# Performance work log

Measured on AMD Instinct MI355X. Metric: run time of the kernel, lower is better.

The kernel has to match this reference:

```python
import jax, jax.numpy as jnp
import numpy as np

K_HOPS = 3
N_NODES = 50000
N_EDGES = 800000
N_FEAT = 256
N_CLASS = 64


def setup_inputs() -> dict:
    key = jax.random.key(0)
    k1, k2, k3, k4 = jax.random.split(key, 4)
    x = jax.random.normal(k1, (N_NODES, N_FEAT), dtype=jnp.float32)
    edge_index = jax.random.randint(k2, (2, N_EDGES), 0, N_NODES, dtype=jnp.int64)
    # Linear(nfeat -> nclass) params, Glorot-ish init
    W = jax.random.normal(k3, (N_FEAT, N_CLASS), dtype=jnp.float32) / np.sqrt(N_FEAT)
    b = jnp.zeros((N_CLASS,), dtype=jnp.float32)
    return {"x": x, "edge_index": edge_index, "W": W, "b": b}


def reference(x, edge_index, W, b):
    # SGC: out = (D^-1/2 (A+I) D^-1/2)^K x  @ W + b
    N = x.shape[0]
    self_idx = jnp.arange(N, dtype=edge_index.dtype)
    src = jnp.concatenate([edge_index[0], self_idx])  # [E+N]
    dst = jnp.concatenate([edge_index[1], self_idx])  # [E+N]
    deg = jax.ops.segment_sum(jnp.ones_like(dst, dtype=x.dtype), dst, num_segments=N)
    dinv = jnp.where(deg > 0, jax.lax.rsqrt(deg), 0.0)
    norm = dinv[src] * dinv[dst]  # [E+N] per-edge coefficient
    for _ in range(K_HOPS):
        # gather source features, scale, scatter-add into destinations
        x = jax.ops.segment_sum(x[src] * norm[:, None], dst, num_segments=N)
    return x @ W + b
```

## Files before the change

### kernel.cpp

```cpp
#include <hip/hip_runtime.h>
#include <hip/hip_bf16.h>


#define NFEAT 256
#define NCLS  64
#define ELLW  64
#define NPB   128
#define BCAP  4096
#define PCHUNK 8192

typedef __attribute__((ext_vector_type(8))) short bf16x8;
typedef __attribute__((ext_vector_type(4))) float f32x4;
typedef __attribute__((ext_vector_type(2))) float f32x2;
typedef __attribute__((ext_vector_type(4))) int   i32x4;
typedef __attribute__((ext_vector_type(4))) unsigned int u32x4;

__device__ __forceinline__ float bf2f(unsigned int u) {
    return __uint_as_float(u << 16);
}
__device__ __forceinline__ float bf2f_hi(unsigned int u) {
    return __uint_as_float(u & 0xffff0000u);
}
__device__ __forceinline__ unsigned short f2bf(float f) {
    unsigned int u = __float_as_uint(f);
    unsigned int r = u + 0x7fffu + ((u >> 16) & 1u);
    return (unsigned short)(r >> 16);
}
__device__ __forceinline__ unsigned int pack2bf(float a, float b) {
    return (unsigned int)f2bf(a) | ((unsigned int)f2bf(b) << 16);
}

__global__ void k_setup(const void* ei, int twoE, int nnodes,
                        const unsigned int* __restrict__ x, int nwords,
                        const void* __restrict__ Wg, const void* __restrict__ Bg,
                        int* flag, int* fflag, int* gcur, int NB,
                        unsigned short* __restrict__ Wt, float* __restrict__ bc) {
    __shared__ int acc;
    const int t = threadIdx.x;
    const int b = blockIdx.x;
    if (t == 0) acc = 0;
    __syncthreads();

    if (b == 0) {
        const long long* p = (const long long*)ei;
        int nchk = 2048;
        if (nchk > twoE / 2) nchk = twoE / 2;
        int bad = 0;
        for (int i = t; i < nchk; i += 256) {
            long long v = p[i];
            if (v < 0 || v >= (long long)nnodes) bad++;
        }
        if (bad) atomicAdd(&acc, bad);
        __syncthreads();
        if (t == 0) *flag = (acc == 0) ? 1 : 0;
        return;
    }

    int lim = nwords < 4096 ? nwords : 4096;
    int wild = 0;
    for (int i = t; i < lim; i += 256) {
        unsigned int lo = x[i] & 0xffffu;
        unsigned int expf = (lo >> 7) & 0xffu;
        if (expf >= 0x97u) wild++;
    }
    if (wild) atomicAdd(&acc, wild);
    __syncthreads();
    const bool isbf = (acc < 8);

    if (b == 1) {
        if (t == 0) *fflag = isbf ? 1 : 0;
        for (int i = t; i < NB; i += 256) gcur[i] = 0;
        if (t < NCLS) {
            bc[t] = isbf ? bf2f(((const unsigned short*)Bg)[t])
                         : ((const float*)Bg)[t];
        }
        return;
    }

    int i = (b - 2) * 256 + t;
    if (i < NFEAT * NCLS) {
        int n = i >> 8, k = i & 255;
        Wt[i] = isbf ? ((const unsigned short*)Wg)[k * NCLS + n]
                     : f2bf(((const float*)Wg)[k * NCLS + n]);
    }
}

__launch_bounds__(256)
__global__ void k_fused(const void* __restrict__ Xg,
                        const unsigned short* __restrict__ Wt,
                        unsigned short* __restrict__ Yb,
                        int N, int NB, const int* __restrict__ fflag,
                        const void* __restrict__ ei, int E, const int* __restrict__ flag,
                        unsigned int* __restrict__ bucket, int* __restrict__ gcur,
                        int ngemm) {
    __shared__ char smem[32768 + 3 * 1600];
    const int t = threadIdx.x;

    if (blockIdx.x >= ngemm) {
        unsigned int* stage = (unsigned int*)smem;
        int* hist = (int*)(smem + 32768);
        int* base = hist + 400;
        int* rank = base + 400;
        for (int b = t; b < NB; b += 256) { hist[b] = 0; rank[b] = 0; }
        __syncthreads();
        const int bstart = (blockIdx.x - ngemm) * PCHUNK;
        const bool is64 = (*flag != 0);
#pragma unroll
        for (int i = 0; i < PCHUNK / 256; ++i) {
            int e = bstart + i * 256 + t;
            unsigned int v = 0xFFFFFFFFu;
            if (e < E) {
                int ss, dd;
                if (is64) {
                    ss = (int)__builtin_nontemporal_load((const long long*)ei + e);
                    dd = (int)__builtin_nontemporal_load((const long long*)ei + E + e);
                } else {
                    ss = __builtin_nontemporal_load((const int*)ei + e);
                    dd = __builtin_nontemporal_load((const int*)ei + E + e);
                }
                int j = dd >> 7;
                atomicAdd(&hist[j], 1);
                v = ((unsigned int)j << 23) | ((unsigned int)(dd & 127) << 16) |
                    (unsigned int)ss;
            }
            stage[i * 256 + t] = v;
        }
        __syncthreads();
        for (int b = t; b < NB; b += 256) base[b] = atomicAdd(&gcur[b], hist[b]);
        __syncthreads();
#pragma unroll
        for (int i = 0; i < PCHUNK / 256; ++i) {
            unsigned int v = stage[i * 256 + t];
            if (v != 0xFFFFFFFFu) {
                int j = v >> 23;
                int r = atomicAdd(&rank[j], 1);
                int pos = base[j] + r;
                if (pos < BCAP)
                    bucket[(size_t)j * BCAP + pos] = v & 0x7FFFFFu;
            }
        }
        return;
    }

    unsigned short* Ws = (unsigned short*)smem;
    for (int it = 0; it < 8; ++it) {
        int idx = t + 256 * it;
        int lane_e = idx & 63;
        int nt = (idx >> 6) & 3;
        int ks = idx >> 8;
        int n = nt * 16 + (lane_e & 15);
        int k = ks * 32 + (lane_e >> 4) * 8;
        const unsigned short* srcp = Wt + n * 256 + k;
        ushort4 v0 = *(const ushort4*)srcp;
        ushort4 v1 = *(const ushort4*)(srcp + 4);
        unsigned short* dstp = &Ws[idx * 8];
        *(ushort4*)dstp = v0;
        *(ushort4*)(dstp + 4) = v1;
    }
    __syncthreads();

    const int wv = t >> 6, lane = t & 63;
    const int m = lane & 15, q = lane >> 4;
    const int row = blockIdx.x * 64 + wv * 16 + m;
    const bool rowok = row < N;
    const bool isbf = (*fflag != 0);

    f32x4 acc0 = {0.f, 0.f, 0.f, 0.f};
    f32x4 acc1 = {0.f, 0.f, 0.f, 0.f};
    f32x4 acc2 = {0.f, 0.f, 0.f, 0.f};
    f32x4 acc3 = {0.f, 0.f, 0.f, 0.f};

    for (int ks = 0; ks < 8; ++ks) {
        const int kk = ks * 32 + q * 8;
        bf16x8 af = {0, 0, 0, 0, 0, 0, 0, 0};
        if (rowok) {
            if (isbf) {
                const i32x4* xp = (const i32x4*)((const unsigned short*)Xg + (size_t)row * NFEAT + kk);
                i32x4 raw = __builtin_nontemporal_load(xp);
#pragma unroll
                for (int h = 0; h < 4; ++h) {
                    af[2 * h]     = (short)(raw[h] & 0xffff);
                    af[2 * h + 1] = (short)(((unsigned int)raw[h]) >> 16);
                }
            } else {
                const i32x4* xp = (const i32x4*)((const float*)Xg + (size_t)row * NFEAT + kk);
                i32x4 r0 = __builtin_nontemporal_load(xp);
                i32x4 r1 = __builtin_nontemporal_load(xp + 1);
#pragma unroll
                for (int h = 0; h < 4; ++h) {
                    af[h]     = (short)f2bf(__int_as_float(r0[h]));
                    af[h + 4] = (short)f2bf(__int_as_float(r1[h]));
                }
            }
        }
        const unsigned short* wbase = &Ws[(ks * 4) * 512 + lane * 8];
        bf16x8 b0 = *(const bf16x8*)(wbase);
        bf16x8 b1 = *(const bf16x8*)(wbase + 512);
        bf16x8 b2 = *(const bf16x8*)(wbase + 1024);
        bf16x8 b3 = *(const bf16x8*)(wbase + 1536);
        acc0 = __builtin_amdgcn_mfma_f32_16x16x32_bf16(af, b0, acc0, 0, 0, 0);
        acc1 = __builtin_amdgcn_mfma_f32_16x16x32_bf16(af, b1, acc1, 0, 0, 0);
        acc2 = __builtin_amdgcn_mfma_f32_16x16x32_bf16(af, b2, acc2, 0, 0, 0);
        acc3 = __builtin_amdgcn_mfma_f32_16x16x32_bf16(af, b3, acc3, 0, 0, 0);
    }

    const int rowbase = blockIdx.x * 64 + wv * 16 + q * 4;
#pragma unroll
    for (int i = 0; i < 4; ++i) {
        int gr = rowbase + i;
        if (gr < N) {
            unsigned short* yp = Yb + (size_t)gr * NCLS + m;
            yp[0]  = f2bf(acc0[i]);
            yp[16] = f2bf(acc1[i]);
            yp[32] = f2bf(acc2[i]);
            yp[48] = f2bf(acc3[i]);
        }
    }
}

__launch_bounds__(256)
__global__ void k_build(const unsigned int* __restrict__ bucket,
                        const int* __restrict__ gcur,
                        int* __restrict__ cnt, float* __restrict__ dinv,
                        unsigned short* __restrict__ ellu,
                        const unsigned int* __restrict__ Yb,
                        unsigned int* __restrict__ Zlo,
                        unsigned int* __restrict__ Zhi,
                        int N) {
    __shared__ unsigned short ellb[NPB * ELLW];
    __shared__ int lcnt[NPB];
    __shared__ float sdinv[NPB];
    const int t = threadIdx.x;
    const int j = blockIdx.x;
    if (t < NPB) lcnt[t] = 0;
    {
        u32x4* eb4 = (u32x4*)ellb;
        u32x4 z = {0, 0, 0, 0};
        for (int i = t; i < NPB * ELLW / 8; i += 256) eb4[i] = z;
    }
    __syncthreads();
    int total = gcur[j];
    if (total > BCAP) total = BCAP;
    const unsigned int* bb = bucket + (size_t)j * BCAP;
    for (int i = t; i < total; i += 256) {
        unsigned int v = __builtin_nontemporal_load(bb + i);
        int ld = (v >> 16) & 127;
        int s = v & 0xffffu;
        int r = atomicAdd(&lcnt[ld], 1);
        if (r < ELLW) ellb[(ld << 6) + r] = (unsigned short)s;
    }
    __syncthreads();
    const int node0 = j << 7;
    if (t < NPB) {
        int node = node0 + t;
        int c = lcnt[t];
        float dv = rsqrtf((float)(c + 1));
        sdinv[t] = dv;
        if (node < N) {
            cnt[node] = c > ELLW ? ELLW : c;
            dinv[node] = dv;
        }
    }
    __syncthreads();
    u32x4* ellg = (u32x4*)ellu;
    const u32x4* eb = (const u32x4*)ellb;
    for (int i = t; i < NPB * (ELLW / 8); i += 256) {
        int node = node0 + (i >> 3);
        if (node < N) ellg[(size_t)node0 * 8 + i] = eb[i];
    }
    for (int w = t; w < NPB * 32; w += 256) {
        int nl = w >> 5, l = w & 31;
        int node = node0 + nl;
        if (node < N) {
            float dv = sdinv[nl];
            unsigned int y = Yb[(size_t)node * 32 + l];
            unsigned int zz = pack2bf(dv * bf2f(y), dv * bf2f_hi(y));
            if (l < 16) Zlo[(size_t)node * 16 + l] = zz;
            else        Zhi[(size_t)node * 16 + (l - 16)] = zz;
        }
    }
}

__launch_bounds__(256)
__global__ void k_hop(const unsigned int* __restrict__ Zlo_in,
                      const unsigned int* __restrict__ Zhi_in,
                      const unsigned short* __restrict__ ellu,
                      const int* __restrict__ cnt, const float* __restrict__ dinv,
                      unsigned int* __restrict__ Zlo_out,
                      unsigned int* __restrict__ Zhi_out,
                      float* __restrict__ outf,
                      const float* __restrict__ bc, int N) {
    const int half = blockIdx.x & 1;
    const int node = (blockIdx.x >> 1) * 16 + (threadIdx.x >> 4);
    if (node >= N) return;
    const int l = threadIdx.x & 15;
    const unsigned int* __restrict__ Zin = half ? Zhi_in : Zlo_in;

    const int deg = __builtin_nontemporal_load(cnt + node);
    const float dn = __builtin_nontemporal_load(dinv + node);
    unsigned int zself = Zin[node * 16 + l];
    float a0 = bf2f(zself), a1 = 0.f, a2 = 0.f, a3 = 0.f;
    float b0 = bf2f_hi(zself), b1 = 0.f, b2 = 0.f, b3 = 0.f;
    const unsigned short* erow = ellu + (size_t)node * ELLW;
    int e = 0;
    for (; e + 16 <= deg; e += 16) {
        u32x4 ua = __builtin_nontemporal_load((const u32x4*)(erow + e));
        u32x4 ub = __builtin_nontemporal_load((const u32x4*)(erow + e) + 1);
        int s[16];
#pragma unroll
        for (int i = 0; i < 4; ++i) {
            s[2 * i]     = (int)(ua[i] & 0xffffu);
            s[2 * i + 1] = (int)(ua[i] >> 16);
            s[2 * i + 8] = (int)(ub[i] & 0xffffu);
            s[2 * i + 9] = (int)(ub[i] >> 16);
        }
        unsigned int z[16];
#pragma unroll
        for (int i = 0; i < 16; ++i) z[i] = Zin[s[i] * 16 + l];
#pragma unroll
        for (int i = 0; i < 16; i += 4) {
            a0 += bf2f(z[i]);     b0 += bf2f_hi(z[i]);
            a1 += bf2f(z[i + 1]); b1 += bf2f_hi(z[i + 1]);
            a2 += bf2f(z[i + 2]); b2 += bf2f_hi(z[i + 2]);
            a3 += bf2f(z[i + 3]); b3 += bf2f_hi(z[i + 3]);
        }
    }
    if (e < deg) {
        u32x4 ua = __builtin_nontemporal_load((const u32x4*)(erow + e));
        u32x4 ub = __builtin_nontemporal_load((const u32x4*)(erow + e) + 1);
        int s[16];
#pragma unroll
        for (int i = 0; i < 4; ++i) {
            s[2 * i]     = (int)(ua[i] & 0xffffu);
            s[2 * i + 1] = (int)(ua[i] >> 16);
            s[2 * i + 8] = (int)(ub[i] & 0xffffu);
            s[2 * i + 9] = (int)(ub[i] >> 16);
        }
        unsigned int z[16];
#pragma unroll
        for (int i = 0; i < 16; ++i) z[i] = Zin[s[i] * 16 + l];
#pragma unroll
        for (int i = 0; i < 16; i += 4) {
            bool g0 = (e + i < deg), g1 = (e + i + 1 < deg);
            bool g2 = (e + i + 2 < deg), g3 = (e + i + 3 < deg);
            a0 += g0 ? bf2f(z[i]) : 0.f;     b0 += g0 ? bf2f_hi(z[i]) : 0.f;
            a1 += g1 ? bf2f(z[i + 1]) : 0.f; b1 += g1 ? bf2f_hi(z[i + 1]) : 0.f;
            a2 += g2 ? bf2f(z[i + 2]) : 0.f; b2 += g2 ? bf2f_hi(z[i + 2]) : 0.f;
            a3 += g3 ? bf2f(z[i + 3]) : 0.f; b3 += g3 ? bf2f_hi(z[i + 3]) : 0.f;
        }
    }
    float lo = (a0 + a1) + (a2 + a3);
    float hi = (b0 + b1) + (b2 + b3);
    if (outf) {
        float2 bv = *(const float2*)(bc + half * 32 + 2 * l);
        f32x2 o = {dn * lo + bv.x, dn * hi + bv.y};
        __builtin_nontemporal_store(o, (f32x2*)(outf + (size_t)node * NCLS + half * 32 + 2 * l));
    } else {
        unsigned int* __restrict__ Zout = half ? Zhi_out : Zlo_out;
        float d2 = dn * dn;
        __builtin_nontemporal_store(pack2bf(d2 * lo, d2 * hi), Zout + (size_t)node * 16 + l);
    }
}

extern "C" void kernel_launch(void* const* d_in, const int* in_sizes, int n_in,
                              void* d_out, int out_size, void* d_ws, size_t ws_size,
                              hipStream_t stream) {
    const void* X  = d_in[0];
    const void* EI = d_in[1];
    const void* W  = d_in[2];
    const void* B  = d_in[3];
    float* out = (float*)d_out;

    const int N = in_sizes[0] / NFEAT;
    const int twoE = in_sizes[1];
    const int E = twoE / 2;
    const int NB = (N + NPB - 1) / NPB;

    char* p = (char*)d_ws;
    auto alloc = [&](size_t bytes) -> char* {
        char* q = p;
        p += (bytes + 255) & ~(size_t)255;
        return q;
    };
    int*   flag   = (int*)alloc(4);
    int*   fflag  = (int*)alloc(4);
    int*   gcur   = (int*)alloc((size_t)NB * 4);
    int*   cnt    = (int*)alloc((size_t)N * 4);
    float* dinv   = (float*)alloc((size_t)N * 4);
    unsigned short* Wt = (unsigned short*)alloc((size_t)NFEAT * NCLS * 2);
    float* bc     = (float*)alloc((size_t)NCLS * 4);
    unsigned int* bucket = (unsigned int*)alloc((size_t)NB * BCAP * 4);
    unsigned short* ellu = (unsigned short*)alloc((size_t)N * ELLW * 2);
    unsigned short* Y0 = (unsigned short*)alloc((size_t)N * NCLS * 2);
    unsigned int* Zlo0 = (unsigned int*)alloc((size_t)N * 16 * 4);
    unsigned int* Zlo1 = (unsigned int*)alloc((size_t)N * 16 * 4);
    unsigned int* Zhi0 = (unsigned int*)alloc((size_t)N * 16 * 4);
    unsigned int* Zhi1 = (unsigned int*)alloc((size_t)N * 16 * 4);

    k_setup<<<2 + NFEAT * NCLS / 256, 256, 0, stream>>>(
        EI, twoE, N, (const unsigned int*)X, in_sizes[0] / 2,
        W, B, flag, fflag, gcur, NB, Wt, bc);

    const int ngemm = (N + 63) / 64;
    const int npart = (E + PCHUNK - 1) / PCHUNK;
    k_fused<<<ngemm + npart, 256, 0, stream>>>(X, Wt, Y0, N, NB, fflag,
                                               EI, E, flag, bucket, gcur, ngemm);

    k_build<<<NB, 256, 0, stream>>>(bucket, gcur, cnt, dinv, ellu,
                                    (const unsigned int*)Y0, Zlo0, Zhi0, N);

    const int nb_h = 2 * ((N + 15) / 16);
    k_hop<<<nb_h, 256, 0, stream>>>(Zlo0, Zhi0, ellu, cnt, dinv,
                                    Zlo1, Zhi1, nullptr, bc, N);
    k_hop<<<nb_h, 256, 0, stream>>>(Zlo1, Zhi1, ellu, cnt, dinv,
                                    Zlo0, Zhi0, nullptr, bc, N);
    k_hop<<<nb_h, 256, 0, stream>>>(Zlo0, Zhi0, ellu, cnt, dinv,
                                    nullptr, nullptr, out, bc, N);
}
```

Baseline: 204.1 us.

## Split hop kernels per feature half and reorder partition blocks first

Each hop is now launched separately for the low and high 32-feature halves, so each launch gathers from a single 1.6MB Z array that fits better in L2/MALL, instead of interleaving both halves in one grid. The edge-partition blocks are moved ahead of the GEMM blocks in the fused launch so they are scheduled first, and the partition chunk size drops to 2048 edges so more, smaller blocks spread the histogram work. The cost is twice as many hop launches and more global atomics on the bucket cursors.

```diff
diff --git a/kernel.cpp b/kernel.cpp
--- a/kernel.cpp
+++ b/kernel.cpp
@@ -7,7 +7,7 @@
 #define ELLW  64
 #define NPB   128
 #define BCAP  4096
-#define PCHUNK 8192
+#define PCHUNK 2048
 
 typedef __attribute__((ext_vector_type(8))) short bf16x8;
 typedef __attribute__((ext_vector_type(4))) float f32x4;
@@ -92,18 +92,18 @@
                         int N, int NB, const int* __restrict__ fflag,
                         const void* __restrict__ ei, int E, const int* __restrict__ flag,
                         unsigned int* __restrict__ bucket, int* __restrict__ gcur,
-                        int ngemm) {
+                        int npart) {
     __shared__ char smem[32768 + 3 * 1600];
     const int t = threadIdx.x;
 
-    if (blockIdx.x >= ngemm) {
+    if (blockIdx.x < npart) {
         unsigned int* stage = (unsigned int*)smem;
         int* hist = (int*)(smem + 32768);
         int* base = hist + 400;
         int* rank = base + 400;
         for (int b = t; b < NB; b += 256) { hist[b] = 0; rank[b] = 0; }
         __syncthreads();
-        const int bstart = (blockIdx.x - ngemm) * PCHUNK;
+        const int bstart = blockIdx.x * PCHUNK;
         const bool is64 = (*flag != 0);
 #pragma unroll
         for (int i = 0; i < PCHUNK / 256; ++i) {
@@ -142,6 +142,7 @@
         return;
     }
 
+    const int gb = blockIdx.x - npart;
     unsigned short* Ws = (unsigned short*)smem;
     for (int it = 0; it < 8; ++it) {
         int idx = t + 256 * it;
@@ -161,7 +162,7 @@
 
     const int wv = t >> 6, lane = t & 63;
     const int m = lane & 15, q = lane >> 4;
-    const int row = blockIdx.x * 64 + wv * 16 + m;
+    const int row = gb * 64 + wv * 16 + m;
     const bool rowok = row < N;
     const bool isbf = (*fflag != 0);
 
@@ -204,7 +205,7 @@
         acc3 = __builtin_amdgcn_mfma_f32_16x16x32_bf16(af, b3, acc3, 0, 0, 0);
     }
 
-    const int rowbase = blockIdx.x * 64 + wv * 16 + q * 4;
+    const int rowbase = gb * 64 + wv * 16 + q * 4;
 #pragma unroll
     for (int i = 0; i < 4; ++i) {
         int gr = rowbase + i;
@@ -282,19 +283,15 @@
 }
 
 __launch_bounds__(256)
-__global__ void k_hop(const unsigned int* __restrict__ Zlo_in,
-                      const unsigned int* __restrict__ Zhi_in,
+__global__ void k_hop(const unsigned int* __restrict__ Zin,
                       const unsigned short* __restrict__ ellu,
                       const int* __restrict__ cnt, const float* __restrict__ dinv,
-                      unsigned int* __restrict__ Zlo_out,
-                      unsigned int* __restrict__ Zhi_out,
+                      unsigned int* __restrict__ Zout,
                       float* __restrict__ outf,
-                      const float* __restrict__ bc, int N) {
-    const int half = blockIdx.x & 1;
-    const int node = (blockIdx.x >> 1) * 16 + (threadIdx.x >> 4);
+                      const float* __restrict__ bc, int N, int half) {
+    const int node = blockIdx.x * 16 + (threadIdx.x >> 4);
     if (node >= N) return;
     const int l = threadIdx.x & 15;
-    const unsigned int* __restrict__ Zin = half ? Zhi_in : Zlo_in;
 
     const int deg = __builtin_nontemporal_load(cnt + node);
     const float dn = __builtin_nontemporal_load(dinv + node);
@@ -356,7 +353,6 @@
         f32x2 o = {dn * lo + bv.x, dn * hi + bv.y};
         __builtin_nontemporal_store(o, (f32x2*)(outf + (size_t)node * NCLS + half * 32 + 2 * l));
     } else {
-        unsigned int* __restrict__ Zout = half ? Zhi_out : Zlo_out;
         float d2 = dn * dn;
         __builtin_nontemporal_store(pack2bf(d2 * lo, d2 * hi), Zout + (size_t)node * 16 + l);
     }
@@ -404,16 +400,16 @@
     const int ngemm = (N + 63) / 64;
     const int npart = (E + PCHUNK - 1) / PCHUNK;
     k_fused<<<ngemm + npart, 256, 0, stream>>>(X, Wt, Y0, N, NB, fflag,
-                                               EI, E, flag, bucket, gcur, ngemm);
+                                               EI, E, flag, bucket, gcur, npart);
 
     k_build<<<NB, 256, 0, stream>>>(bucket, gcur, cnt, dinv, ellu,
                                     (const unsigned int*)Y0, Zlo0, Zhi0, N);
 
-    const int nb_h = 2 * ((N + 15) / 16);
-    k_hop<<<nb_h, 256, 0, stream>>>(Zlo0, Zhi0, ellu, cnt, dinv,
-                                    Zlo1, Zhi1, nullptr, bc, N);
-    k_hop<<<nb_h, 256, 0, stream>>>(Zlo1, Zhi1, ellu, cnt, dinv,
-                                    Zlo0, Zhi0, nullptr, bc, N);
-    k_hop<<<nb_h, 256, 0, stream>>>(Zlo0, Zhi0, ellu, cnt, dinv,
-                                    nullptr, nullptr, out, bc, N);
-}
+    const int nb_h = (N + 15) / 16;
+    k_hop<<<nb_h, 256, 0, stream>>>(Zlo0, ellu, cnt, dinv, Zlo1, nullptr, bc, N, 0);
+    k_hop<<<nb_h, 256, 0, stream>>>(Zhi0, ellu, cnt, dinv, Zhi1, nullptr, bc, N, 1);
+    k_hop<<<nb_h, 256, 0, stream>>>(Zlo1, ellu, cnt, dinv, Zlo0, nullptr, bc, N, 0);
+    k_hop<<<nb_h, 256, 0, stream>>>(Zhi1, ellu, cnt, dinv, Zhi0, nullptr, bc, N, 1);
+    k_hop<<<nb_h, 256, 0, stream>>>(Zlo0, ellu, cnt, dinv, nullptr, out, bc, N, 0);
+    k_hop<<<nb_h, 256, 0, stream>>>(Zhi0, ellu, cnt, dinv, nullptr, out, bc, N, 1);
+}
```

New measurement: 212.4 us. +4.1%, slower.
